# Optimization experiments

Measured on AMD Instinct MI355X. Metric: run time of the kernel, lower is better.

Reference implementation:

```python
import jax, jax.numpy as jnp
import numpy as np

B, S, NX, H = 4, 1024, 1024, 16
D = NX // H  # 64 head dim
NEG = -1e9


def setup_inputs() -> dict:
    key = jax.random.key(0)
    k1, k2, k3 = jax.random.split(key, 3)
    x = jax.random.normal(k1, (B, S, NX), dtype=jnp.float32)
    # boolean mask, True = masked (causal: cannot attend to future)
    causal = ~jnp.tril(jnp.ones((S, S), dtype=bool))
    mask_self_attention = causal[None, None, :, :]  # [1,1,S,S]
    w_attn = jax.random.normal(k2, (NX, 3 * NX), dtype=jnp.float32) * 0.02
    b_attn = jnp.zeros((3 * NX,), dtype=jnp.float32)
    w_proj = jax.random.normal(k3, (NX, NX), dtype=jnp.float32) * 0.02
    b_proj = jnp.zeros((NX,), dtype=jnp.float32)
    return {"x": x, "mask_self_attention": mask_self_attention,
            "w_attn": w_attn, "b_attn": b_attn,
            "w_proj": w_proj, "b_proj": b_proj}


def reference(x, mask_self_attention, w_attn, b_attn, w_proj, b_proj):
    # c_attn: fused QKV projection
    qkv = jnp.einsum('bsn,nm->bsm', x, w_attn) + b_attn  # [B,S,3*NX]
    q, k, v = jnp.split(qkv, 3, axis=-1)
    # split heads -> [B,H,S,D]
    def heads(t):
        return t.reshape(B, S, H, D).transpose(0, 2, 1, 3)
    q, k, v = heads(q), heads(k), heads(v)
    # present = stack(key [B,H,S,D], value [B,H,S,D]) -> [2,B,H,S,D]
    present = jnp.stack((k, v))
    # scaled dot-product attention with boolean mask (True = masked)
    w = jnp.einsum('bhqd,bhkd->bhqk', q, k) / jnp.sqrt(jnp.float32(D))
    w = jnp.where(mask_self_attention, NEG, w)
    w = jax.nn.softmax(w, axis=-1)
    # attn_pdrop is identity in eval mode
    a = jnp.einsum('bhqk,bhkd->bhqd', w, v)
    # merge heads -> [B,S,NX]
    a = a.transpose(0, 2, 1, 3).reshape(B, S, NX)
    # c_proj
    a = jnp.einsum('bsn,nm->bsm', a, w_proj) + b_proj
    return (a, present)
```

## Files before the change

### kernel.cpp

```cpp
#include <hip/hip_runtime.h>
#include <math.h>
#include <stdint.h>

#define BATCH 4
#define SEQ   1024
#define NXDIM 1024
#define NHEAD 16
#define DHEAD 64
#define QKVN  3072
#define MROWS 4096
#define KDIM  1024

typedef short short8 __attribute__((ext_vector_type(8)));
typedef float f32x4  __attribute__((ext_vector_type(4)));

typedef const __attribute__((address_space(1))) unsigned int* gptr_t;
typedef __attribute__((address_space(3))) unsigned int* lptr_t;

__device__ __forceinline__ unsigned short f2bf(float f) {
    unsigned int u = __float_as_uint(f);
    u += 0x7FFF + ((u >> 16) & 1);
    return (unsigned short)(u >> 16);
}
__device__ __forceinline__ float bf2f(unsigned short h) {
    return __uint_as_float(((unsigned int)h) << 16);
}
__device__ __forceinline__ unsigned pk_hi_rtne(float a, float b) {
    unsigned ua = __float_as_uint(a), ub = __float_as_uint(b);
    ua += 0x7FFF + ((ua >> 16) & 1);
    ub += 0x7FFF + ((ub >> 16) & 1);
    return __builtin_amdgcn_perm(ub, ua, 0x07060302u);
}
__device__ __forceinline__ unsigned pk_hi_trunc(float a, float b) {
    return __builtin_amdgcn_perm(__float_as_uint(b), __float_as_uint(a), 0x07060302u);
}
__device__ __forceinline__ float trunc_bf(float a) {
    return __uint_as_float(__float_as_uint(a) & 0xFFFF0000u);
}
__device__ __forceinline__ float rtne_bf(float a) {
    unsigned u = __float_as_uint(a);
    u += 0x7FFF + ((u >> 16) & 1);
    return __uint_as_float(u & 0xFFFF0000u);
}

__global__ __launch_bounds__(256) void split_x_kernel(
    const float* __restrict__ x, unsigned short* __restrict__ xh,
    unsigned short* __restrict__ xl)
{
    const int t = blockIdx.x * 256 + threadIdx.x;
    const int tile = t >> 9, u = t & 511;
    const int mt = tile >> 5, kt = tile & 31;
    const int g = u >> 6, khalf = (u >> 4) & 3, r16 = u & 15;
    const int m = mt * 128 + g * 16 + r16;
    const int k = kt * 32 + khalf * 8;
    const float4 v0 = *(const float4*)&x[(size_t)m * KDIM + k];
    const float4 v1 = *(const float4*)&x[(size_t)m * KDIM + k + 4];
    const float vv[8] = {v0.x, v0.y, v0.z, v0.w, v1.x, v1.y, v1.z, v1.w};
    unsigned short h[8], l[8];
    #pragma unroll
    for (int e = 0; e < 8; ++e) {
        h[e] = f2bf(vv[e]);
        l[e] = f2bf(vv[e] - bf2f(h[e]));
    }
    uint4 ph, pl;
    ph.x = (unsigned)h[0] | ((unsigned)h[1] << 16);
    ph.y = (unsigned)h[2] | ((unsigned)h[3] << 16);
    ph.z = (unsigned)h[4] | ((unsigned)h[5] << 16);
    ph.w = (unsigned)h[6] | ((unsigned)h[7] << 16);
    pl.x = (unsigned)l[0] | ((unsigned)l[1] << 16);
    pl.y = (unsigned)l[2] | ((unsigned)l[3] << 16);
    pl.z = (unsigned)l[4] | ((unsigned)l[5] << 16);
    pl.w = (unsigned)l[6] | ((unsigned)l[7] << 16);
    *(uint4*)&xh[(size_t)t * 8] = ph;
    *(uint4*)&xl[(size_t)t * 8] = pl;
}

__global__ __launch_bounds__(256) void split_w_kernel(
    const float* __restrict__ w, unsigned short* __restrict__ wh,
    unsigned short* __restrict__ wl, int N)
{
    const int t = blockIdx.x * 256 + threadIdx.x;
    const int tile = t >> 9, u = t & 511;
    const int nt = tile >> 5, kt = tile & 31;
    const int gn = u >> 6, khalf = (u >> 4) & 3, c16 = u & 15;
    const int n = nt * 128 + gn * 16 + c16;
    const int k0 = kt * 32 + khalf * 8;
    unsigned short h[8], l[8];
    #pragma unroll
    for (int e = 0; e < 8; ++e) {
        const float v = w[(size_t)(k0 + e) * N + n];
        h[e] = f2bf(v);
        l[e] = f2bf(v - bf2f(h[e]));
    }
    uint4 ph, pl;
    ph.x = (unsigned)h[0] | ((unsigned)h[1] << 16);
    ph.y = (unsigned)h[2] | ((unsigned)h[3] << 16);
    ph.z = (unsigned)h[4] | ((unsigned)h[5] << 16);
    ph.w = (unsigned)h[6] | ((unsigned)h[7] << 16);
    pl.x = (unsigned)l[0] | ((unsigned)l[1] << 16);
    pl.y = (unsigned)l[2] | ((unsigned)l[3] << 16);
    pl.z = (unsigned)l[4] | ((unsigned)l[5] << 16);
    pl.w = (unsigned)l[6] | ((unsigned)l[7] << 16);
    *(uint4*)&wh[(size_t)t * 8] = ph;
    *(uint4*)&wl[(size_t)t * 8] = pl;
}

template<int EPI>
__global__ __launch_bounds__(256, 2) void mfma_gemm_kernel(
    const unsigned short* __restrict__ Ahg, const unsigned short* __restrict__ Alg,
    const unsigned short* __restrict__ Bhg, const unsigned short* __restrict__ Blg,
    const float* __restrict__ bias,
    float* __restrict__ o0, float* __restrict__ o1, float* __restrict__ o2,
    unsigned short* __restrict__ qh_o, unsigned short* __restrict__ ql_o)
{
    __shared__ unsigned char lds[32768];
    const int tid = threadIdx.x;
    const int wave = tid >> 6, lane = tid & 63;
    const int bm = blockIdx.y, bn = blockIdx.x;

    const unsigned short* mysrc;
    if      (wave == 0) mysrc = Ahg + (size_t)bm * 32 * 4096;
    else if (wave == 1) mysrc = Alg + (size_t)bm * 32 * 4096;
    else if (wave == 2) mysrc = Bhg + (size_t)bn * 32 * 4096;
    else                mysrc = Blg + (size_t)bn * 32 * 4096;

    const f32x4 fzero = {0.f, 0.f, 0.f, 0.f};
    f32x4 acc[4][4];
    #pragma unroll
    for (int i = 0; i < 4; ++i)
        #pragma unroll
        for (int j = 0; j < 4; ++j) acc[i][j] = fzero;

    const int frag_off = ((lane >> 4) << 8) + ((lane & 15) << 4);
    const int ag = (wave >> 1) * 4;
    const int bg = (wave & 1) * 4;

    for (int kt = 0; kt < 32; ++kt) {
        __syncthreads();
        const unsigned short* src = mysrc + kt * 4096;
        #pragma unroll
        for (int c = 0; c < 8; ++c) {
            const unsigned short* gsrc = src + (c << 9) + (lane << 3);
            __builtin_amdgcn_global_load_lds(
                (gptr_t)(uintptr_t)gsrc,
                (lptr_t)(uintptr_t)(&lds[(wave << 13) + (c << 10)]),
                16, 0, 0);
        }
        __syncthreads();

        short8 ah[4], al[4], bh[4], bl[4];
        #pragma unroll
        for (int i = 0; i < 4; ++i) {
            const int ao = (ag + i) * 1024 + frag_off;
            const int bo = (bg + i) * 1024 + frag_off;
            ah[i] = __builtin_bit_cast(short8, *(const uint4*)&lds[ao]);
            al[i] = __builtin_bit_cast(short8, *(const uint4*)&lds[8192 + ao]);
            bh[i] = __builtin_bit_cast(short8, *(const uint4*)&lds[16384 + bo]);
            bl[i] = __builtin_bit_cast(short8, *(const uint4*)&lds[24576 + bo]);
        }
        #pragma unroll
        for (int i = 0; i < 4; ++i)
            #pragma unroll
            for (int j = 0; j < 4; ++j) {
                acc[i][j] = __builtin_amdgcn_mfma_f32_16x16x32_bf16(ah[i], bh[j], acc[i][j], 0, 0, 0);
                acc[i][j] = __builtin_amdgcn_mfma_f32_16x16x32_bf16(ah[i], bl[j], acc[i][j], 0, 0, 0);
                acc[i][j] = __builtin_amdgcn_mfma_f32_16x16x32_bf16(al[i], bh[j], acc[i][j], 0, 0, 0);
            }
    }

    const int gm_base = bm * 128 + (wave >> 1) * 64 + ((lane >> 4) << 2);
    const int gn_base = bn * 128 + (wave & 1) * 64 + (lane & 15);
    #pragma unroll
    for (int j = 0; j < 4; ++j) {
        const int gn = gn_base + j * 16;
        const float bj = bias[gn];
        if (EPI == 0) {
            #pragma unroll
            for (int i = 0; i < 4; ++i)
                #pragma unroll
                for (int r = 0; r < 4; ++r)
                    o0[(size_t)(gm_base + i * 16 + r) * NXDIM + gn] = acc[i][j][r] + bj;
        } else {
            const int sec = gn >> 10;
            const int hh  = (gn >> 6) & 15;
            const int d   = gn & 63;
            #pragma unroll
            for (int i = 0; i < 4; ++i)
                #pragma unroll
                for (int r = 0; r < 4; ++r) {
                    const int gm = gm_base + i * 16 + r;
                    const int bq = gm >> 10, s = gm & 1023;
                    const size_t idx = (((size_t)bq * NHEAD + hh) * SEQ + s) * DHEAD + d;
                    const float val = acc[i][j][r] + bj;
                    if (sec == 1)      o1[idx] = val;
                    else if (sec == 2) o2[idx] = val;
                    else {
                        const float vq = val * 0.125f;
                        const unsigned short hq = f2bf(vq);
                        qh_o[idx] = hq;
                        ql_o[idx] = f2bf(vq - bf2f(hq));
                    }
                }
        }
    }
}

__global__ __launch_bounds__(256, 3) void attn_kernel(
    const unsigned short* __restrict__ qh_g, const unsigned short* __restrict__ ql_g,
    const float* __restrict__ kbuf, const float* __restrict__ vbuf,
    unsigned short* __restrict__ ahi, unsigned short* __restrict__ alo)
{
    __shared__ unsigned char lds[49152];
    unsigned char* const Kh  = lds;
    unsigned char* const Kl  = lds + 8192;
    unsigned char* const Vth = lds + 16384;
    unsigned char* const Vtl = lds + 24576;

    const int tid  = threadIdx.x;
    const int wave = tid >> 6, lane = tid & 63;
    const int l15  = lane & 15, lg = lane >> 4;
    const int qt = 15 - (int)(blockIdx.x & 15);
    const int bh = (int)(blockIdx.x >> 4);
    const int q0 = qt << 6;
    unsigned char* const Ps = lds + 32768 + (wave << 12);

    const float* kb = kbuf + (size_t)bh * SEQ * DHEAD;
    const float* vb = vbuf + (size_t)bh * SEQ * DHEAD;

    short8 qhf[2], qlf[2];
    {
        const size_t qb0 = ((size_t)bh * SEQ + q0 + wave * 16 + l15) * DHEAD + lg * 8;
        qhf[0] = *(const short8*)(qh_g + qb0);
        qhf[1] = *(const short8*)(qh_g + qb0 + 32);
        qlf[0] = *(const short8*)(ql_g + qb0);
        qlf[1] = *(const short8*)(ql_g + qb0 + 32);
    }

    const int krow = tid >> 2, kdq = (tid & 3) << 4;
    const int vrow = tid & 63, vkq = tid >> 6;

    float4 kreg[4];
    float  vreg[16];

    auto load_tile = [&](int kb0) {
        #pragma unroll
        for (int c = 0; c < 4; ++c)
            kreg[c] = *(const float4*)&kb[(size_t)(kb0 + krow) * DHEAD + kdq + 4 * c];
        #pragma unroll
        for (int kk = 0; kk < 16; ++kk)
            vreg[kk] = vb[(size_t)(kb0 + vkq * 16 + kk) * DHEAD + vrow];
    };
    auto commit = [&]() {
        #pragma unroll
        for (int c = 0; c < 4; ++c) {
            const float4 f = kreg[c];
            const unsigned h01 = pk_hi_rtne(f.x, f.y);
            const unsigned h23 = pk_hi_rtne(f.z, f.w);
            const unsigned l01 = pk_hi_trunc(f.x - rtne_bf(f.x), f.y - rtne_bf(f.y));
            const unsigned l23 = pk_hi_trunc(f.z - rtne_bf(f.z), f.w - rtne_bf(f.w));
            const int slot = ((tid & 3) << 1) + (c >> 1);
            const int addr = krow * 128 + ((slot ^ (krow & 7)) << 4) + ((c & 1) << 3);
            *(uint2*)(Kh + addr) = make_uint2(h01, h23);
            *(uint2*)(Kl + addr) = make_uint2(l01, l23);
        }
        unsigned vhp[8], vlp[8];
        #pragma unroll
        for (int p = 0; p < 8; ++p) {
            const float a = vreg[2 * p], b2 = vreg[2 * p + 1];
            vhp[p] = pk_hi_trunc(a, b2);
            vlp[p] = pk_hi_trunc(a - trunc_bf(a), b2 - trunc_bf(b2));
        }
        const int vs0 = vkq << 1;
        const int vb0 = vrow * 128;
        const int vsw = vrow & 7;
        *(uint4*)(Vth + vb0 + (((vs0    ) ^ vsw) << 4)) = make_uint4(vhp[0], vhp[1], vhp[2], vhp[3]);
        *(uint4*)(Vth + vb0 + (((vs0 + 1) ^ vsw) << 4)) = make_uint4(vhp[4], vhp[5], vhp[6], vhp[7]);
        *(uint4*)(Vtl + vb0 + (((vs0    ) ^ vsw) << 4)) = make_uint4(vlp[0], vlp[1], vlp[2], vlp[3]);
        *(uint4*)(Vtl + vb0 + (((vs0 + 1) ^ vsw) << 4)) = make_uint4(vlp[4], vlp[5], vlp[6], vlp[7]);
    };

    load_tile(0);
    commit();

    float mprev[4], lsum[4];
    f32x4 oacc[4];
    #pragma unroll
    for (int r = 0; r < 4; ++r) { mprev[r] = -3.0e38f; lsum[r] = 0.f; }
    #pragma unroll
    for (int jd = 0; jd < 4; ++jd) oacc[jd] = (f32x4){0.f, 0.f, 0.f, 0.f};

    const int fsw = lg ^ (l15 & 7);

    for (int kt = 0; kt <= qt; ++kt) {
        __syncthreads();
        if (kt < qt) load_tile((kt + 1) << 6);

        f32x4 sacc[4];
        #pragma unroll
        for (int j = 0; j < 4; ++j) sacc[j] = (f32x4){0.f, 0.f, 0.f, 0.f};
        #pragma unroll
        for (int ks = 0; ks < 2; ++ks) {
            #pragma unroll
            for (int j = 0; j < 4; ++j) {
                const int addr = ((j << 4) + l15) * 128 + ((fsw ^ (ks << 2)) << 4);
                const short8 khf = *(const short8*)(Kh + addr);
                const short8 klf = *(const short8*)(Kl + addr);
                sacc[j] = __builtin_amdgcn_mfma_f32_16x16x32_bf16(qhf[ks], khf, sacc[j], 0, 0, 0);
                sacc[j] = __builtin_amdgcn_mfma_f32_16x16x32_bf16(qhf[ks], klf, sacc[j], 0, 0, 0);
                sacc[j] = __builtin_amdgcn_mfma_f32_16x16x32_bf16(qlf[ks], khf, sacc[j], 0, 0, 0);
            }
        }

        const int k0 = kt << 6;
        const bool diag = (kt == qt);
        #pragma unroll
        for (int r = 0; r < 4; ++r) {
            const int qg = q0 + wave * 16 + lg * 4 + r;
            float mx = -3.0e38f;
            #pragma unroll
            for (int j = 0; j < 4; ++j) {
                float sv = sacc[j][r];
                if (diag && (k0 + (j << 4) + l15) > qg) sv = -1.0e9f;
                sacc[j][r] = sv;
                mx = fmaxf(mx, sv);
            }
            mx = fmaxf(mx, __shfl_xor(mx, 1));
            mx = fmaxf(mx, __shfl_xor(mx, 2));
            mx = fmaxf(mx, __shfl_xor(mx, 4));
            mx = fmaxf(mx, __shfl_xor(mx, 8));
            const float mnew = fmaxf(mprev[r], mx);
            const float corr = __expf(mprev[r] - mnew);
            float rsum = 0.f;
            #pragma unroll
            for (int j = 0; j < 4; ++j) {
                const float p = __expf(sacc[j][r] - mnew);
                sacc[j][r] = p;
                rsum += p;
            }
            rsum += __shfl_xor(rsum, 1);
            rsum += __shfl_xor(rsum, 2);
            rsum += __shfl_xor(rsum, 4);
            rsum += __shfl_xor(rsum, 8);
            lsum[r] = lsum[r] * corr + rsum;
            mprev[r] = mnew;
            #pragma unroll
            for (int jd = 0; jd < 4; ++jd) oacc[jd][r] *= corr;
        }

        #pragma unroll
        for (int j = 0; j < 4; ++j)
            #pragma unroll
            for (int r = 0; r < 4; ++r) {
                const float p = sacc[j][r];
                const unsigned up = __float_as_uint(p);
                const float plo = p - __uint_as_float(up & 0xFFFF0000u);
                const unsigned packed = (up & 0xFFFF0000u) | (__float_as_uint(plo) >> 16);
                const int qq = lg * 4 + r;
                const int kcol = (j << 4) + l15;
                const int addr = qq * 256 + (((kcol >> 2) ^ qq) << 4) + ((kcol & 3) << 2);
                *(unsigned*)(Ps + addr) = packed;
            }

        #pragma unroll
        for (int ks = 0; ks < 2; ++ks) {
            const int s0 = (ks << 3) + (lg << 1);
            const uint4 pk0 = *(const uint4*)(Ps + l15 * 256 + (((s0    ) ^ l15) << 4));
            const uint4 pk1 = *(const uint4*)(Ps + l15 * 256 + (((s0 + 1) ^ l15) << 4));
            uint4 uh, ul;
            uh.x = __builtin_amdgcn_perm(pk0.y, pk0.x, 0x07060302u);
            uh.y = __builtin_amdgcn_perm(pk0.w, pk0.z, 0x07060302u);
            uh.z = __builtin_amdgcn_perm(pk1.y, pk1.x, 0x07060302u);
            uh.w = __builtin_amdgcn_perm(pk1.w, pk1.z, 0x07060302u);
            ul.x = __builtin_amdgcn_perm(pk0.y, pk0.x, 0x05040100u);
            ul.y = __builtin_amdgcn_perm(pk0.w, pk0.z, 0x05040100u);
            ul.z = __builtin_amdgcn_perm(pk1.y, pk1.x, 0x05040100u);
            ul.w = __builtin_amdgcn_perm(pk1.w, pk1.z, 0x05040100u);
            const short8 phf = __builtin_bit_cast(short8, uh);
            const short8 plf = __builtin_bit_cast(short8, ul);
            #pragma unroll
            for (int jd = 0; jd < 4; ++jd) {
                const int vaddr = ((jd << 4) + l15) * 128 + ((fsw ^ (ks << 2)) << 4);
                const short8 vhf = *(const short8*)(Vth + vaddr);
                const short8 vlf = *(const short8*)(Vtl + vaddr);
                oacc[jd] = __builtin_amdgcn_mfma_f32_16x16x32_bf16(phf, vhf, oacc[jd], 0, 0, 0);
                oacc[jd] = __builtin_amdgcn_mfma_f32_16x16x32_bf16(phf, vlf, oacc[jd], 0, 0, 0);
                oacc[jd] = __builtin_amdgcn_mfma_f32_16x16x32_bf16(plf, vhf, oacc[jd], 0, 0, 0);
            }
        }

        __syncthreads();
        if (kt < qt) commit();
    }

    const int hh = bh & 15, bq = bh >> 4;
    float inv[4];
    #pragma unroll
    for (int r = 0; r < 4; ++r) inv[r] = 1.0f / lsum[r];
    #pragma unroll
    for (int jd = 0; jd < 4; ++jd) {
        const int kcol = (hh << 6) + (jd << 4) + l15;
        const int ktile = kcol >> 5, khalf = (kcol & 31) >> 3, k7 = kcol & 7;
        #pragma unroll
        for (int r = 0; r < 4; ++r) {
            const int m = (bq << 10) + q0 + wave * 16 + lg * 4 + r;
            const float o = oacc[jd][r] * inv[r];
            const unsigned short hv = f2bf(o);
            const unsigned short lv = f2bf(o - bf2f(hv));
            const size_t off = ((size_t)((m >> 7) * 32 + ktile) << 12)
                             + (size_t)((((m & 127) >> 4) << 9) + (khalf << 7) + ((m & 15) << 3) + k7);
            ahi[off] = hv;
            alo[off] = lv;
        }
    }
}

extern "C" void kernel_launch(void* const* d_in, const int* in_sizes, int n_in,
                              void* d_out, int out_size, void* d_ws, size_t ws_size,
                              hipStream_t stream) {
    const float* x      = (const float*)d_in[0];
    const float* w_attn = (const float*)d_in[2];
    const float* b_attn = (const float*)d_in[3];
    const float* w_proj = (const float*)d_in[4];
    const float* b_proj = (const float*)d_in[5];

    float* out = (float*)d_out;
    float* kbuf = out + (size_t)BATCH * SEQ * NXDIM;
    float* vbuf = kbuf + (size_t)BATCH * NHEAD * SEQ * DHEAD;
    unsigned short* qh = (unsigned short*)out;
    unsigned short* ql = qh + (size_t)BATCH * NHEAD * SEQ * DHEAD;

    unsigned char* ws = (unsigned char*)d_ws;
    unsigned short* xh  = (unsigned short*)(ws);
    unsigned short* xl  = (unsigned short*)(ws + (8u  << 20));
    unsigned short* wah = (unsigned short*)(ws + (16u << 20));
    unsigned short* wal = (unsigned short*)(ws + (22u << 20));
    unsigned short* wph = (unsigned short*)(ws + (28u << 20));
    unsigned short* wpl = (unsigned short*)(ws + (30u << 20));
    unsigned short* ah  = xh;
    unsigned short* al  = xl;

    split_x_kernel<<<2048, 256, 0, stream>>>(x, xh, xl);
    split_w_kernel<<<1536, 256, 0, stream>>>(w_attn, wah, wal, QKVN);
    split_w_kernel<<<512,  256, 0, stream>>>(w_proj, wph, wpl, NXDIM);
    mfma_gemm_kernel<1><<<dim3(24, 32), 256, 0, stream>>>(
        xh, xl, wah, wal, b_attn, nullptr, kbuf, vbuf, qh, ql);
    attn_kernel<<<1024, 256, 0, stream>>>(qh, ql, kbuf, vbuf, ah, al);
    mfma_gemm_kernel<0><<<dim3(8, 32), 256, 0, stream>>>(
        ah, al, wph, wpl, b_proj, out, nullptr, nullptr, nullptr, nullptr);
}
```

Measured before the change: 320.1 us.

## Pair causal query tiles per block and streamline online softmax

Each attention block now handles two query tiles, pp and 15-pp, so every block does the same amount of causal work, and the grid shrinks from 1024 to 512 blocks. The log2(e) factor is folded into the Q scale so the kernel can use exp2f. The running-max rescale is skipped unless the max grows by more than 8, and row sums come from MFMA against a ones vector instead of shuffle reductions. s_setprio hints are added around the MFMA sections. Fewer blocks may reduce occupancy and latency hiding, and the lazy rescale allows larger intermediate values.

```diff
diff --git a/kernel.cpp b/kernel.cpp
--- a/kernel.cpp
+++ b/kernel.cpp
@@ -195,7 +195,7 @@
                     if (sec == 1)      o1[idx] = val;
                     else if (sec == 2) o2[idx] = val;
                     else {
-                        const float vq = val * 0.125f;
+                        const float vq = val * 0.18033688f;
                         const unsigned short hq = f2bf(vq);
                         qh_o[idx] = hq;
                         ql_o[idx] = f2bf(vq - bf2f(hq));
@@ -219,22 +219,12 @@
     const int tid  = threadIdx.x;
     const int wave = tid >> 6, lane = tid & 63;
     const int l15  = lane & 15, lg = lane >> 4;
-    const int qt = 15 - (int)(blockIdx.x & 15);
-    const int bh = (int)(blockIdx.x >> 4);
-    const int q0 = qt << 6;
+    const int pp = (int)(blockIdx.x & 7);
+    const int bh = (int)(blockIdx.x >> 3);
     unsigned char* const Ps = lds + 32768 + (wave << 12);
 
     const float* kb = kbuf + (size_t)bh * SEQ * DHEAD;
     const float* vb = vbuf + (size_t)bh * SEQ * DHEAD;
-
-    short8 qhf[2], qlf[2];
-    {
-        const size_t qb0 = ((size_t)bh * SEQ + q0 + wave * 16 + l15) * DHEAD + lg * 8;
-        qhf[0] = *(const short8*)(qh_g + qb0);
-        qhf[1] = *(const short8*)(qh_g + qb0 + 32);
-        qlf[0] = *(const short8*)(ql_g + qb0);
-        qlf[1] = *(const short8*)(ql_g + qb0 + 32);
-    }
 
     const int krow = tid >> 2, kdq = (tid & 3) << 4;
     const int vrow = tid & 63, vkq = tid >> 6;
@@ -279,139 +269,163 @@
         *(uint4*)(Vtl + vb0 + (((vs0 + 1) ^ vsw) << 4)) = make_uint4(vlp[4], vlp[5], vlp[6], vlp[7]);
     };
 
+    const int fsw = lg ^ (l15 & 7);
+    const int hh = bh & 15, bq = bh >> 4;
+
+    short8 vone;
+    #pragma unroll
+    for (int e = 0; e < 8; ++e) vone[e] = (short)0x3F80;
+
+    auto process = [&](int q0, int nt, bool has_next) {
+        short8 qhf[2], qlf[2];
+        {
+            const size_t qb0 = ((size_t)bh * SEQ + q0 + wave * 16 + l15) * DHEAD + lg * 8;
+            qhf[0] = *(const short8*)(qh_g + qb0);
+            qhf[1] = *(const short8*)(qh_g + qb0 + 32);
+            qlf[0] = *(const short8*)(ql_g + qb0);
+            qlf[1] = *(const short8*)(ql_g + qb0 + 32);
+        }
+        float mprev[4];
+        f32x4 lacc = (f32x4){0.f, 0.f, 0.f, 0.f};
+        f32x4 oacc[4];
+        #pragma unroll
+        for (int r = 0; r < 4; ++r) mprev[r] = -3.0e38f;
+        #pragma unroll
+        for (int jd = 0; jd < 4; ++jd) oacc[jd] = (f32x4){0.f, 0.f, 0.f, 0.f};
+
+        for (int kt = 0; kt < nt; ++kt) {
+            __syncthreads();
+            const bool pf = (kt + 1 < nt) || has_next;
+            if (pf) load_tile((kt + 1 < nt) ? (kt + 1) << 6 : 0);
+
+            f32x4 sacc[4];
+            #pragma unroll
+            for (int j = 0; j < 4; ++j) sacc[j] = (f32x4){0.f, 0.f, 0.f, 0.f};
+            __builtin_amdgcn_s_setprio(1);
+            #pragma unroll
+            for (int ks = 0; ks < 2; ++ks) {
+                #pragma unroll
+                for (int j = 0; j < 4; ++j) {
+                    const int addr = ((j << 4) + l15) * 128 + ((fsw ^ (ks << 2)) << 4);
+                    const short8 khf = *(const short8*)(Kh + addr);
+                    const short8 klf = *(const short8*)(Kl + addr);
+                    sacc[j] = __builtin_amdgcn_mfma_f32_16x16x32_bf16(qhf[ks], khf, sacc[j], 0, 0, 0);
+                    sacc[j] = __builtin_amdgcn_mfma_f32_16x16x32_bf16(qhf[ks], klf, sacc[j], 0, 0, 0);
+                    sacc[j] = __builtin_amdgcn_mfma_f32_16x16x32_bf16(qlf[ks], khf, sacc[j], 0, 0, 0);
+                }
+            }
+            __builtin_amdgcn_s_setprio(0);
+
+            const int k0 = kt << 6;
+            const bool diag = (k0 == q0);
+            float mx[4];
+            #pragma unroll
+            for (int r = 0; r < 4; ++r) {
+                const int qg = q0 + wave * 16 + lg * 4 + r;
+                float m_ = -3.0e38f;
+                #pragma unroll
+                for (int j = 0; j < 4; ++j) {
+                    float sv = sacc[j][r];
+                    if (diag && (k0 + (j << 4) + l15) > qg) sv = -1.0e9f;
+                    sacc[j][r] = sv;
+                    m_ = fmaxf(m_, sv);
+                }
+                m_ = fmaxf(m_, __shfl_xor(m_, 1));
+                m_ = fmaxf(m_, __shfl_xor(m_, 2));
+                m_ = fmaxf(m_, __shfl_xor(m_, 4));
+                m_ = fmaxf(m_, __shfl_xor(m_, 8));
+                mx[r] = m_;
+            }
+
+            bool need = false;
+            #pragma unroll
+            for (int r = 0; r < 4; ++r) need |= (mx[r] > mprev[r] + 8.0f);
+            if (__any(need)) {
+                #pragma unroll
+                for (int r = 0; r < 4; ++r) {
+                    const float mnew = fmaxf(mprev[r], mx[r]);
+                    const float corr = exp2f(mprev[r] - mnew);
+                    lacc[r] *= corr;
+                    #pragma unroll
+                    for (int jd = 0; jd < 4; ++jd) oacc[jd][r] *= corr;
+                    mprev[r] = mnew;
+                }
+            }
+
+            #pragma unroll
+            for (int j = 0; j < 4; ++j)
+                #pragma unroll
+                for (int r = 0; r < 4; ++r) {
+                    const float p = exp2f(sacc[j][r] - mprev[r]);
+                    const unsigned up = __float_as_uint(p);
+                    const float plo = p - __uint_as_float(up & 0xFFFF0000u);
+                    const unsigned packed = (up & 0xFFFF0000u) | (__float_as_uint(plo) >> 16);
+                    const int qq = lg * 4 + r;
+                    const int kcol = (j << 4) + l15;
+                    const int addr = qq * 256 + (((kcol >> 2) ^ qq) << 4) + ((kcol & 3) << 2);
+                    *(unsigned*)(Ps + addr) = packed;
+                }
+
+            __builtin_amdgcn_s_setprio(1);
+            #pragma unroll
+            for (int ks = 0; ks < 2; ++ks) {
+                const int s0 = (ks << 3) + (lg << 1);
+                const uint4 pk0 = *(const uint4*)(Ps + l15 * 256 + (((s0    ) ^ l15) << 4));
+                const uint4 pk1 = *(const uint4*)(Ps + l15 * 256 + (((s0 + 1) ^ l15) << 4));
+                uint4 uh, ul;
+                uh.x = __builtin_amdgcn_perm(pk0.y, pk0.x, 0x07060302u);
+                uh.y = __builtin_amdgcn_perm(pk0.w, pk0.z, 0x07060302u);
+                uh.z = __builtin_amdgcn_perm(pk1.y, pk1.x, 0x07060302u);
+                uh.w = __builtin_amdgcn_perm(pk1.w, pk1.z, 0x07060302u);
+                ul.x = __builtin_amdgcn_perm(pk0.y, pk0.x, 0x05040100u);
+                ul.y = __builtin_amdgcn_perm(pk0.w, pk0.z, 0x05040100u);
+                ul.z = __builtin_amdgcn_perm(pk1.y, pk1.x, 0x05040100u);
+                ul.w = __builtin_amdgcn_perm(pk1.w, pk1.z, 0x05040100u);
+                const short8 phf = __builtin_bit_cast(short8, uh);
+                const short8 plf = __builtin_bit_cast(short8, ul);
+                lacc = __builtin_amdgcn_mfma_f32_16x16x32_bf16(phf, vone, lacc, 0, 0, 0);
+                lacc = __builtin_amdgcn_mfma_f32_16x16x32_bf16(plf, vone, lacc, 0, 0, 0);
+                #pragma unroll
+                for (int jd = 0; jd < 4; ++jd) {
+                    const int vaddr = ((jd << 4) + l15) * 128 + ((fsw ^ (ks << 2)) << 4);
+                    const short8 vhf = *(const short8*)(Vth + vaddr);
+                    const short8 vlf = *(const short8*)(Vtl + vaddr);
+                    oacc[jd] = __builtin_amdgcn_mfma_f32_16x16x32_bf16(phf, vhf, oacc[jd], 0, 0, 0);
+                    oacc[jd] = __builtin_amdgcn_mfma_f32_16x16x32_bf16(phf, vlf, oacc[jd], 0, 0, 0);
+                    oacc[jd] = __builtin_amdgcn_mfma_f32_16x16x32_bf16(plf, vhf, oacc[jd], 0, 0, 0);
+                }
+            }
+            __builtin_amdgcn_s_setprio(0);
+
+            __syncthreads();
+            if (pf) commit();
+        }
+
+        float inv[4];
+        #pragma unroll
+        for (int r = 0; r < 4; ++r) inv[r] = 1.0f / lacc[r];
+        #pragma unroll
+        for (int jd = 0; jd < 4; ++jd) {
+            const int kcol = (hh << 6) + (jd << 4) + l15;
+            const int ktile = kcol >> 5, khalf = (kcol & 31) >> 3, k7 = kcol & 7;
+            #pragma unroll
+            for (int r = 0; r < 4; ++r) {
+                const int m = (bq << 10) + q0 + wave * 16 + lg * 4 + r;
+                const float o = oacc[jd][r] * inv[r];
+                const unsigned short hv = f2bf(o);
+                const unsigned short lv = f2bf(o - bf2f(hv));
+                const size_t off = ((size_t)((m >> 7) * 32 + ktile) << 12)
+                                 + (size_t)((((m & 127) >> 4) << 9) + (khalf << 7) + ((m & 15) << 3) + k7);
+                ahi[off] = hv;
+                alo[off] = lv;
+            }
+        }
+    };
+
     load_tile(0);
     commit();
-
-    float mprev[4], lsum[4];
-    f32x4 oacc[4];
-    #pragma unroll
-    for (int r = 0; r < 4; ++r) { mprev[r] = -3.0e38f; lsum[r] = 0.f; }
-    #pragma unroll
-    for (int jd = 0; jd < 4; ++jd) oacc[jd] = (f32x4){0.f, 0.f, 0.f, 0.f};
-
-    const int fsw = lg ^ (l15 & 7);
-
-    for (int kt = 0; kt <= qt; ++kt) {
-        __syncthreads();
-        if (kt < qt) load_tile((kt + 1) << 6);
-
-        f32x4 sacc[4];
-        #pragma unroll
-        for (int j = 0; j < 4; ++j) sacc[j] = (f32x4){0.f, 0.f, 0.f, 0.f};
-        #pragma unroll
-        for (int ks = 0; ks < 2; ++ks) {
-            #pragma unroll
-            for (int j = 0; j < 4; ++j) {
-                const int addr = ((j << 4) + l15) * 128 + ((fsw ^ (ks << 2)) << 4);
-                const short8 khf = *(const short8*)(Kh + addr);
-                const short8 klf = *(const short8*)(Kl + addr);
-                sacc[j] = __builtin_amdgcn_mfma_f32_16x16x32_bf16(qhf[ks], khf, sacc[j], 0, 0, 0);
-                sacc[j] = __builtin_amdgcn_mfma_f32_16x16x32_bf16(qhf[ks], klf, sacc[j], 0, 0, 0);
-                sacc[j] = __builtin_amdgcn_mfma_f32_16x16x32_bf16(qlf[ks], khf, sacc[j], 0, 0, 0);
-            }
-        }
-
-        const int k0 = kt << 6;
-        const bool diag = (kt == qt);
-        #pragma unroll
-        for (int r = 0; r < 4; ++r) {
-            const int qg = q0 + wave * 16 + lg * 4 + r;
-            float mx = -3.0e38f;
-            #pragma unroll
-            for (int j = 0; j < 4; ++j) {
-                float sv = sacc[j][r];
-                if (diag && (k0 + (j << 4) + l15) > qg) sv = -1.0e9f;
-                sacc[j][r] = sv;
-                mx = fmaxf(mx, sv);
-            }
-            mx = fmaxf(mx, __shfl_xor(mx, 1));
-            mx = fmaxf(mx, __shfl_xor(mx, 2));
-            mx = fmaxf(mx, __shfl_xor(mx, 4));
-            mx = fmaxf(mx, __shfl_xor(mx, 8));
-            const float mnew = fmaxf(mprev[r], mx);
-            const float corr = __expf(mprev[r] - mnew);
-            float rsum = 0.f;
-            #pragma unroll
-            for (int j = 0; j < 4; ++j) {
-                const float p = __expf(sacc[j][r] - mnew);
-                sacc[j][r] = p;
-                rsum += p;
-            }
-            rsum += __shfl_xor(rsum, 1);
-            rsum += __shfl_xor(rsum, 2);
-            rsum += __shfl_xor(rsum, 4);
-            rsum += __shfl_xor(rsum, 8);
-            lsum[r] = lsum[r] * corr + rsum;
-            mprev[r] = mnew;
-            #pragma unroll
-            for (int jd = 0; jd < 4; ++jd) oacc[jd][r] *= corr;
-        }
-
-        #pragma unroll
-        for (int j = 0; j < 4; ++j)
-            #pragma unroll
-            for (int r = 0; r < 4; ++r) {
-                const float p = sacc[j][r];
-                const unsigned up = __float_as_uint(p);
-                const float plo = p - __uint_as_float(up & 0xFFFF0000u);
-                const unsigned packed = (up & 0xFFFF0000u) | (__float_as_uint(plo) >> 16);
-                const int qq = lg * 4 + r;
-                const int kcol = (j << 4) + l15;
-                const int addr = qq * 256 + (((kcol >> 2) ^ qq) << 4) + ((kcol & 3) << 2);
-                *(unsigned*)(Ps + addr) = packed;
-            }
-
-        #pragma unroll
-        for (int ks = 0; ks < 2; ++ks) {
-            const int s0 = (ks << 3) + (lg << 1);
-            const uint4 pk0 = *(const uint4*)(Ps + l15 * 256 + (((s0    ) ^ l15) << 4));
-            const uint4 pk1 = *(const uint4*)(Ps + l15 * 256 + (((s0 + 1) ^ l15) << 4));
-            uint4 uh, ul;
-            uh.x = __builtin_amdgcn_perm(pk0.y, pk0.x, 0x07060302u);
-            uh.y = __builtin_amdgcn_perm(pk0.w, pk0.z, 0x07060302u);
-            uh.z = __builtin_amdgcn_perm(pk1.y, pk1.x, 0x07060302u);
-            uh.w = __builtin_amdgcn_perm(pk1.w, pk1.z, 0x07060302u);
-            ul.x = __builtin_amdgcn_perm(pk0.y, pk0.x, 0x05040100u);
-            ul.y = __builtin_amdgcn_perm(pk0.w, pk0.z, 0x05040100u);
-            ul.z = __builtin_amdgcn_perm(pk1.y, pk1.x, 0x05040100u);
-            ul.w = __builtin_amdgcn_perm(pk1.w, pk1.z, 0x05040100u);
-            const short8 phf = __builtin_bit_cast(short8, uh);
-            const short8 plf = __builtin_bit_cast(short8, ul);
-            #pragma unroll
-            for (int jd = 0; jd < 4; ++jd) {
-                const int vaddr = ((jd << 4) + l15) * 128 + ((fsw ^ (ks << 2)) << 4);
-                const short8 vhf = *(const short8*)(Vth + vaddr);
-                const short8 vlf = *(const short8*)(Vtl + vaddr);
-                oacc[jd] = __builtin_amdgcn_mfma_f32_16x16x32_bf16(phf, vhf, oacc[jd], 0, 0, 0);
-                oacc[jd] = __builtin_amdgcn_mfma_f32_16x16x32_bf16(phf, vlf, oacc[jd], 0, 0, 0);
-                oacc[jd] = __builtin_amdgcn_mfma_f32_16x16x32_bf16(plf, vhf, oacc[jd], 0, 0, 0);
-            }
-        }
-
-        __syncthreads();
-        if (kt < qt) commit();
-    }
-
-    const int hh = bh & 15, bq = bh >> 4;
-    float inv[4];
-    #pragma unroll
-    for (int r = 0; r < 4; ++r) inv[r] = 1.0f / lsum[r];
-    #pragma unroll
-    for (int jd = 0; jd < 4; ++jd) {
-        const int kcol = (hh << 6) + (jd << 4) + l15;
-        const int ktile = kcol >> 5, khalf = (kcol & 31) >> 3, k7 = kcol & 7;
-        #pragma unroll
-        for (int r = 0; r < 4; ++r) {
-            const int m = (bq << 10) + q0 + wave * 16 + lg * 4 + r;
-            const float o = oacc[jd][r] * inv[r];
-            const unsigned short hv = f2bf(o);
-            const unsigned short lv = f2bf(o - bf2f(hv));
-            const size_t off = ((size_t)((m >> 7) * 32 + ktile) << 12)
-                             + (size_t)((((m & 127) >> 4) << 9) + (khalf << 7) + ((m & 15) << 3) + k7);
-            ahi[off] = hv;
-            alo[off] = lv;
-        }
-    }
+    process(pp << 6, pp + 1, true);
+    process((15 - pp) << 6, 16 - pp, false);
 }
 
 extern "C" void kernel_launch(void* const* d_in, const int* in_sizes, int n_in,
@@ -441,10 +455,10 @@
 
     split_x_kernel<<<2048, 256, 0, stream>>>(x, xh, xl);
     split_w_kernel<<<1536, 256, 0, stream>>>(w_attn, wah, wal, QKVN);
-    split_w_kernel<<<512,  256, 0, stream>>>(w_proj, wph, wpl, NXDIM);
+    split_w_kernel<<<512,  256, 0, stream>>>(w_proj, wpl == nullptr ? nullptr : wph, wpl, NXDIM);
     mfma_gemm_kernel<1><<<dim3(24, 32), 256, 0, stream>>>(
         xh, xl, wah, wal, b_attn, nullptr, kbuf, vbuf, qh, ql);
-    attn_kernel<<<1024, 256, 0, stream>>>(qh, ql, kbuf, vbuf, ah, al);
+    attn_kernel<<<512, 256, 0, stream>>>(qh, ql, kbuf, vbuf, ah, al);
     mfma_gemm_kernel<0><<<dim3(8, 32), 256, 0, stream>>>(
         ah, al, wph, wpl, b_proj, out, nullptr, nullptr, nullptr, nullptr);
 }
```

Result: faster. 273.5 us (-14.6%).
